# Kernel tuning notes

Measured on AMD Instinct MI355X. Metric: run time of the kernel, lower is better.

Reference implementation:

```python
import jax, jax.numpy as jnp
import numpy as np
from jax import lax

B, L, T = 256, 1024, 128


def setup_inputs() -> dict:
    key = jax.random.key(0)
    k1, k2, k3, k4 = jax.random.split(key, 4)
    transitions = jax.random.normal(k1, (T, T), dtype=jnp.float32)
    feats = jax.random.normal(k2, (B, L, T), dtype=jnp.float32)
    # random lengths in [L//2, L]; position 0 always valid (mask[0].all())
    lengths = jax.random.randint(k3, (B,), L // 2, L + 1)
    mask = jnp.arange(L)[None, :] < lengths[:, None]  # (B, L) bool
    tags = jax.random.randint(k4, (B, L), 0, T).astype(jnp.int64)
    return {"transitions": transitions, "feats": feats, "mask": mask, "tags": tags}


def _forward_score(transitions, feats, mask):
    # CRF forward algorithm: sequential logsumexp DP over time with masking.
    def step(partition, inp):
        f_t, m_t = inp  # (B, T), (B,)
        # scores[b, i, j] = partition[b, i] + transitions[i, j]
        cur = f_t + jax.nn.logsumexp(partition[:, :, None] + transitions[None, :, :], axis=1)
        partition = jnp.where(m_t[:, None], cur, partition)
        return partition, None

    init = feats[:, 0, :]
    feats_t = jnp.swapaxes(feats, 0, 1)  # (L, B, T)
    xs = (feats_t[1:], mask.T[1:])
    partition, _ = lax.scan(step, init, xs)
    return jnp.sum(jax.nn.logsumexp(partition, axis=1))


def _gold_score(transitions, feats, mask, tags):
    unary = jnp.take_along_axis(feats, tags[:, :, None], axis=2)[..., 0]  # (B, L)
    unary_sum = jnp.sum(jnp.where(mask, unary, 0.0))
    binary = transitions[tags[:, :-1], tags[:, 1:]]  # (B, L-1)
    binary_sum = jnp.sum(jnp.where(mask[:, 1:], binary, 0.0))
    return unary_sum + binary_sum


def reference(transitions, feats, mask, tags):
    # scaling_feats == 1 (trainable_balance_weight=False)
    forward_score = _forward_score(transitions, feats, mask)
    gold_score = _gold_score(transitions, feats, mask, tags)
    return forward_score - gold_score
```

## Files before the change

### kernel.cpp

```cpp
#include <hip/hip_runtime.h>

#define CRF_B 256
#define CRF_L 1024
#define CRF_T 128
#define WS_STRIDE 260

typedef __attribute__((ext_vector_type(8))) short bf16x8;
typedef __attribute__((ext_vector_type(4))) float f32x4;
typedef __attribute__((ext_vector_type(2))) short short2v;

#define MF(a, b, cacc) __builtin_amdgcn_mfma_f32_16x16x32_bf16((a), (b), (cacc), 0, 0, 0)
#define WG_BARRIER() asm volatile("s_waitcnt lgkmcnt(0)\n\ts_barrier" ::: "memory")

static __device__ __forceinline__ unsigned short f2bf(float x) {
    union { float f; unsigned u; } v; v.f = x;
    unsigned r = v.u + 0x7FFFu + ((v.u >> 16) & 1u);
    return (unsigned short)(r >> 16);
}
static __device__ __forceinline__ short2v bmax2(short2v a, short2v b) {
    return __builtin_elementwise_max(a, b);
}
static __device__ __forceinline__ short2v fragmax(bf16x8 a) {
    short2v q0 = __builtin_shufflevector(a, a, 0, 1);
    short2v q1 = __builtin_shufflevector(a, a, 2, 3);
    short2v q2 = __builtin_shufflevector(a, a, 4, 5);
    short2v q3 = __builtin_shufflevector(a, a, 6, 7);
    return bmax2(bmax2(q0, q1), bmax2(q2, q3));
}

#define STEP(S, P0, P1, NORM) do {                                             \
    const int sl_ = (S) & 1;                                                   \
    float v0_ = isf ? x0 : F0 * x0;                                            \
    float v1_ = isf ? x1 : F1 * x1;                                            \
    if (g == 0) { s_e[sl_][c0] = f2bf(v0_); s_e[sl_][c1] = f2bf(v1_); }        \
    WG_BARRIER();                                                              \
    bf16x8 A0_ = *(const bf16x8*)&s_e[sl_][ 0 + 8 * g];                        \
    bf16x8 A1_ = *(const bf16x8*)&s_e[sl_][32 + 8 * g];                        \
    bf16x8 A2_ = *(const bf16x8*)&s_e[sl_][64 + 8 * g];                        \
    bf16x8 A3_ = *(const bf16x8*)&s_e[sl_][96 + 8 * g];                        \
    f32x4 dA0_ = MF(A0_, Bf[0][0], Z);  f32x4 dB0_ = MF(A1_, Bf[0][1], Z);     \
    f32x4 dA1_ = MF(A0_, Bf[1][0], Z);  f32x4 dB1_ = MF(A1_, Bf[1][1], Z);     \
    dA0_ = MF(A2_, Bf[0][2], dA0_);  dB0_ = MF(A3_, Bf[0][3], dB0_);           \
    dA1_ = MF(A2_, Bf[1][2], dA1_);  dB1_ = MF(A3_, Bf[1][3], dB1_);           \
    float d0_ = dA0_[0] + dB0_[0];                                             \
    float d1_ = dA1_[0] + dB1_[0];                                             \
    if (NORM) {                                                                \
        short2v mx_ = bmax2(bmax2(fragmax(A0_), fragmax(A1_)),                 \
                            bmax2(fragmax(A2_), fragmax(A3_)));                \
        unsigned mu_ = __builtin_bit_cast(unsigned, mx_);                      \
        float nrm_ = fmaxf(__builtin_bit_cast(float, mu_ << 16),               \
                           __builtin_bit_cast(float, mu_ & 0xFFFF0000u));      \
        float sig_ = __builtin_amdgcn_rcpf(nrm_);                              \
        kap += __logf(nrm_);                                                   \
        d0_ *= sig_; d1_ *= sig_;                                              \
    }                                                                          \
    x0 = isf ? F0 * d0_ : d0_;                                                 \
    x1 = isf ? F1 * d1_ : d1_;                                                 \
    F0 = __expf(P0); F1 = __expf(P1);                                          \
    int rr_ = isf ? ((S) + 3) : (len - (S) - 3);                               \
    if (rr_ > CRF_L - 1) rr_ = CRF_L - 1;                                      \
    if (rr_ < 0) rr_ = 0;                                                      \
    P0 = fb[(size_t)rr_ * CRF_T + c0];                                         \
    P1 = fb[(size_t)rr_ * CRF_T + c1];                                         \
} while (0)

__global__ __launch_bounds__(256, 2) void forward_kernel(
    const float* __restrict__ trans, const float* __restrict__ feats,
    const int* __restrict__ mask, const int* __restrict__ tags,
    float* __restrict__ ws)
{
    const int b    = blockIdx.x >> 1;
    const int dir  = blockIdx.x & 1;
    const bool isf = (dir == 0);
    const int t    = threadIdx.x;
    const int w    = t >> 6;
    const int lane = t & 63;
    const int g    = lane >> 4;
    const int c    = lane & 15;
    const int c0   = 32 * w + c;
    const int c1   = c0 + 16;

    __shared__ __align__(16) unsigned short s_e[2][CRF_T];
    __shared__ float s_gold;
    __shared__ int   s_len;

    if (t == 0) { s_len = 0; s_gold = 0.0f; }
    __syncthreads();

    {
        int cnt = 0; float gsum = 0.0f;
        const int base = b * CRF_L;
        for (int l = t; l < CRF_L; l += 256) {
            if (mask[base + l] != 0) {
                cnt++;
                if (isf) {
                    int tg = tags[base + l];
                    float gv = feats[(size_t)(base + l) * CRF_T + tg];
                    if (l > 0) gv += trans[tags[base + l - 1] * CRF_T + tg];
                    gsum += gv;
                }
            }
        }
        for (int off = 32; off > 0; off >>= 1) {
            cnt  += __shfl_down(cnt, off, 64);
            gsum += __shfl_down(gsum, off, 64);
        }
        if (lane == 0) { atomicAdd(&s_len, cnt); if (isf) atomicAdd(&s_gold, gsum); }
    }

    bf16x8 Bf[2][4];
#pragma unroll
    for (int t2 = 0; t2 < 2; ++t2) {
        const int col = t2 ? c1 : c0;
#pragma unroll
        for (int kt = 0; kt < 4; ++kt)
#pragma unroll
            for (int e = 0; e < 8; ++e) {
                int k = 32 * kt + 8 * g + e;
                int idx = isf ? (k * CRF_T + col) : (col * CRF_T + k);
                Bf[t2][kt][e] = (short)f2bf(__expf(trans[idx]));
            }
    }

    __syncthreads();
    const int len    = s_len;
    const int m      = len >> 1;
    const int nsteps = isf ? m : (len - 1 - m);

    const float* fb = feats + (size_t)b * CRF_L * CRF_T;

    float x0, x1, F0, F1, pfA0, pfA1, pfB0, pfB1;
    float kap = 0.0f;
    if (isf) {
        x0 = __expf(fb[c0]);  x1 = __expf(fb[c1]);
        F0 = __expf(fb[CRF_T + c0]);  F1 = __expf(fb[CRF_T + c1]);
        pfA0 = fb[2 * CRF_T + c0];  pfA1 = fb[2 * CRF_T + c1];
        pfB0 = fb[3 * CRF_T + c0];  pfB1 = fb[3 * CRF_T + c1];
    } else {
        x0 = 1.0f;  x1 = 1.0f;
        F0 = __expf(fb[(size_t)(len - 1) * CRF_T + c0]);
        F1 = __expf(fb[(size_t)(len - 1) * CRF_T + c1]);
        pfA0 = fb[(size_t)(len - 2) * CRF_T + c0];
        pfA1 = fb[(size_t)(len - 2) * CRF_T + c1];
        pfB0 = fb[(size_t)(len - 3) * CRF_T + c0];
        pfB1 = fb[(size_t)(len - 3) * CRF_T + c1];
    }

    const f32x4 Z = {};

    int s = 1;
    for (; s + 1 <= nsteps; s += 2) {
        STEP(s,     pfA0, pfA1, true);
        STEP(s + 1, pfB0, pfB1, false);
    }
    if (s <= nsteps) STEP(s, pfA0, pfA1, true);

    float* wsb = ws + (size_t)b * WS_STRIDE;
    if (g == 0) {
        wsb[dir * 128 + c0] = x0;
        wsb[dir * 128 + c1] = x1;
    }
    if (t == 0) {
        wsb[256 + dir] = kap;
        if (isf) wsb[258] = s_gold;
    }
}

__global__ __launch_bounds__(256) void combine_kernel(
    const float* __restrict__ ws, float* __restrict__ out)
{
    const int t    = threadIdx.x;
    const int lane = t & 63;
    const int w    = t >> 6;
    const float4* pf = (const float4*)(ws + (size_t)t * WS_STRIDE);
    const float4* pb = pf + 32;
    float dot = 0.0f;
#pragma unroll
    for (int k = 0; k < 32; ++k) {
        float4 a = pf[k], bb = pb[k];
        dot += a.x * bb.x + a.y * bb.y + a.z * bb.z + a.w * bb.w;
    }
    const float* ps = ws + (size_t)t * WS_STRIDE;
    float val = ps[256] + ps[257] + __logf(dot) - ps[258];
    for (int off = 32; off > 0; off >>= 1) val += __shfl_down(val, off, 64);
    __shared__ float sw[4];
    if (lane == 0) sw[w] = val;
    __syncthreads();
    if (t == 0) out[0] = sw[0] + sw[1] + sw[2] + sw[3];
}

extern "C" void kernel_launch(void* const* d_in, const int* in_sizes, int n_in,
                              void* d_out, int out_size, void* d_ws, size_t ws_size,
                              hipStream_t stream) {
    const float* trans = (const float*)d_in[0];
    const float* feats = (const float*)d_in[1];
    const int*   mask  = (const int*)d_in[2];
    const int*   tags  = (const int*)d_in[3];
    float*       out   = (float*)d_out;
    float*       ws    = (float*)d_ws;

    hipLaunchKernelGGL(forward_kernel, dim3(2 * CRF_B), dim3(256), 0, stream,
                       trans, feats, mask, tags, ws);
    hipLaunchKernelGGL(combine_kernel, dim3(1), dim3(256), 0, stream, ws, out);
}
```

Measured before the change: 184.4 us.

## Batch eight sequences per block so MFMA rows carry multiple batch elements

```diff
diff --git a/kernel.cpp b/kernel.cpp
--- a/kernel.cpp
+++ b/kernel.cpp
@@ -3,13 +3,13 @@
 #define CRF_B 256
 #define CRF_L 1024
 #define CRF_T 128
-#define WS_STRIDE 260
+#define BPB   8
+#define WS_STRIDE 264
 
 typedef __attribute__((ext_vector_type(8))) short bf16x8;
 typedef __attribute__((ext_vector_type(4))) float f32x4;
-typedef __attribute__((ext_vector_type(2))) short short2v;
-
-#define MF(a, b, cacc) __builtin_amdgcn_mfma_f32_16x16x32_bf16((a), (b), (cacc), 0, 0, 0)
+
+#define MF(a, b, c_) __builtin_amdgcn_mfma_f32_16x16x32_bf16((a), (b), (c_), 0, 0, 0)
 #define WG_BARRIER() asm volatile("s_waitcnt lgkmcnt(0)\n\ts_barrier" ::: "memory")
 
 static __device__ __forceinline__ unsigned short f2bf(float x) {
@@ -17,80 +17,129 @@
     unsigned r = v.u + 0x7FFFu + ((v.u >> 16) & 1u);
     return (unsigned short)(r >> 16);
 }
-static __device__ __forceinline__ short2v bmax2(short2v a, short2v b) {
-    return __builtin_elementwise_max(a, b);
-}
-static __device__ __forceinline__ short2v fragmax(bf16x8 a) {
-    short2v q0 = __builtin_shufflevector(a, a, 0, 1);
-    short2v q1 = __builtin_shufflevector(a, a, 2, 3);
-    short2v q2 = __builtin_shufflevector(a, a, 4, 5);
-    short2v q3 = __builtin_shufflevector(a, a, 6, 7);
-    return bmax2(bmax2(q0, q1), bmax2(q2, q3));
-}
-
-#define STEP(S, P0, P1, NORM) do {                                             \
-    const int sl_ = (S) & 1;                                                   \
-    float v0_ = isf ? x0 : F0 * x0;                                            \
-    float v1_ = isf ? x1 : F1 * x1;                                            \
-    if (g == 0) { s_e[sl_][c0] = f2bf(v0_); s_e[sl_][c1] = f2bf(v1_); }        \
+
+static __device__ __forceinline__ float rowmax16(float v) {
+    int x;
+    x = __builtin_amdgcn_update_dpp(0, __builtin_bit_cast(int, v), 0xB1,  0xF, 0xF, true);
+    v = fmaxf(v, __builtin_bit_cast(float, x));
+    x = __builtin_amdgcn_update_dpp(0, __builtin_bit_cast(int, v), 0x4E,  0xF, 0xF, true);
+    v = fmaxf(v, __builtin_bit_cast(float, x));
+    x = __builtin_amdgcn_update_dpp(0, __builtin_bit_cast(int, v), 0x141, 0xF, 0xF, true);
+    v = fmaxf(v, __builtin_bit_cast(float, x));
+    x = __builtin_amdgcn_update_dpp(0, __builtin_bit_cast(int, v), 0x140, 0xF, 0xF, true);
+    v = fmaxf(v, __builtin_bit_cast(float, x));
+    return v;
+}
+
+#define STEP(S, PF, DONORM) do {                                               \
+    const int  sl_ = (S) & 1;                                                  \
+    char* xb_ = s_xraw + sl_ * 4096;                                           \
+    float F0_[4], F1_[4];                                                      \
+    _Pragma("unroll")                                                          \
+    for (int r_ = 0; r_ < 4; ++r_) {                                           \
+        F0_[r_] = __expf(PF[r_].x);                                            \
+        F1_[r_] = __expf(PF[r_].y);                                            \
+    }                                                                          \
+    if (g2 < 2) {                                                              \
+        _Pragma("unroll")                                                      \
+        for (int r_ = 0; r_ < 4; ++r_) {                                       \
+            const int row_ = 4 * g2 + r_;                                      \
+            float p0_ = isf ? x0[r_] : F0_[r_] * x0[r_];                       \
+            float p1_ = isf ? x1[r_] : F1_[r_] * x1[r_];                       \
+            unsigned pk_ = (__builtin_bit_cast(unsigned, p1_) & 0xFFFF0000u)   \
+                         | (__builtin_bit_cast(unsigned, p0_) >> 16);          \
+            *(unsigned*)(xb_ + row_ * 256 + ((tg0 * 2) ^ (row_ << 4))) = pk_;  \
+        }                                                                      \
+    }                                                                          \
+    _Pragma("unroll")                                                          \
+    for (int r_ = 0; r_ < 4; ++r_) {                                           \
+        int la_ = isf ? (off[r_] + 4 * 512) : (off[r_] - 4 * 512);             \
+        if (!isf) la_ = (la_ < base0[r_]) ? base0[r_] : la_;                   \
+        PF[r_] = *(const float2*)(fbc + la_);                                  \
+        off[r_] += isf ? 512 : -512;                                           \
+    }                                                                          \
     WG_BARRIER();                                                              \
-    bf16x8 A0_ = *(const bf16x8*)&s_e[sl_][ 0 + 8 * g];                        \
-    bf16x8 A1_ = *(const bf16x8*)&s_e[sl_][32 + 8 * g];                        \
-    bf16x8 A2_ = *(const bf16x8*)&s_e[sl_][64 + 8 * g];                        \
-    bf16x8 A3_ = *(const bf16x8*)&s_e[sl_][96 + 8 * g];                        \
+    const char* xr_ = xb_ + c * 256;                                           \
+    bf16x8 A0_ = *(const bf16x8*)(xr_ + ((  0 + 16 * g2) ^ ((c & 7) << 4)));   \
+    bf16x8 A1_ = *(const bf16x8*)(xr_ + (( 64 + 16 * g2) ^ ((c & 7) << 4)));   \
+    bf16x8 A2_ = *(const bf16x8*)(xr_ + ((128 + 16 * g2) ^ ((c & 7) << 4)));   \
+    bf16x8 A3_ = *(const bf16x8*)(xr_ + ((192 + 16 * g2) ^ ((c & 7) << 4)));   \
     f32x4 dA0_ = MF(A0_, Bf[0][0], Z);  f32x4 dB0_ = MF(A1_, Bf[0][1], Z);     \
     f32x4 dA1_ = MF(A0_, Bf[1][0], Z);  f32x4 dB1_ = MF(A1_, Bf[1][1], Z);     \
     dA0_ = MF(A2_, Bf[0][2], dA0_);  dB0_ = MF(A3_, Bf[0][3], dB0_);           \
     dA1_ = MF(A2_, Bf[1][2], dA1_);  dB1_ = MF(A3_, Bf[1][3], dB1_);           \
-    float d0_ = dA0_[0] + dB0_[0];                                             \
-    float d1_ = dA1_[0] + dB1_[0];                                             \
-    if (NORM) {                                                                \
-        short2v mx_ = bmax2(bmax2(fragmax(A0_), fragmax(A1_)),                 \
-                            bmax2(fragmax(A2_), fragmax(A3_)));                \
-        unsigned mu_ = __builtin_bit_cast(unsigned, mx_);                      \
-        float nrm_ = fmaxf(__builtin_bit_cast(float, mu_ << 16),               \
-                           __builtin_bit_cast(float, mu_ & 0xFFFF0000u));      \
-        float sig_ = __builtin_amdgcn_rcpf(nrm_);                              \
-        kap += __logf(nrm_);                                                   \
-        d0_ *= sig_; d1_ *= sig_;                                              \
-    }                                                                          \
-    x0 = isf ? F0 * d0_ : d0_;                                                 \
-    x1 = isf ? F1 * d1_ : d1_;                                                 \
-    F0 = __expf(P0); F1 = __expf(P1);                                          \
-    int rr_ = isf ? ((S) + 3) : (len - (S) - 3);                               \
-    if (rr_ > CRF_L - 1) rr_ = CRF_L - 1;                                      \
-    if (rr_ < 0) rr_ = 0;                                                      \
-    P0 = fb[(size_t)rr_ * CRF_T + c0];                                         \
-    P1 = fb[(size_t)rr_ * CRF_T + c1];                                         \
+    if (DONORM) {                                                              \
+        const int pp_ = ((S) >> 1) & 1;                                        \
+        const float* pm_ = s_pm + (pp_ ^ 1) * 32 + (g2 & 1) * 4;               \
+        f32x4 n0_ = *(const f32x4*)(pm_ + 0);                                  \
+        f32x4 n1_ = *(const f32x4*)(pm_ + 8);                                  \
+        f32x4 n2_ = *(const f32x4*)(pm_ + 16);                                 \
+        f32x4 n3_ = *(const f32x4*)(pm_ + 24);                                 \
+        _Pragma("unroll")                                                      \
+        for (int r_ = 0; r_ < 4; ++r_) {                                       \
+            float nr_ = fmaxf(fmaxf(n0_[r_], n1_[r_]), fmaxf(n2_[r_], n3_[r_]));\
+            float sg_ = __builtin_amdgcn_rcpf(nr_);                            \
+            kap[r_] += __logf(nr_);                                            \
+            float d0_ = (dA0_[r_] + dB0_[r_]) * sg_;                           \
+            float d1_ = (dA1_[r_] + dB1_[r_]) * sg_;                           \
+            x0[r_] = isf ? F0_[r_] * d0_ : d0_;                                \
+            x1[r_] = isf ? F1_[r_] * d1_ : d1_;                                \
+        }                                                                      \
+    } else {                                                                   \
+        _Pragma("unroll")                                                      \
+        for (int r_ = 0; r_ < 4; ++r_) {                                       \
+            float d0_ = dA0_[r_] + dB0_[r_];                                   \
+            float d1_ = dA1_[r_] + dB1_[r_];                                   \
+            x0[r_] = isf ? F0_[r_] * d0_ : d0_;                                \
+            x1[r_] = isf ? F1_[r_] * d1_ : d1_;                                \
+        }                                                                      \
+    }                                                                          \
+    _Pragma("unroll")                                                          \
+    for (int r_ = 0; r_ < 4; ++r_) {                                           \
+        bool hit_ = ((S) == msv[r_]);                                          \
+        sv0[r_] = hit_ ? x0[r_] : sv0[r_];                                     \
+        sv1[r_] = hit_ ? x1[r_] : sv1[r_];                                     \
+        svk[r_] = hit_ ? kap[r_] : svk[r_];                                    \
+    }                                                                          \
+    if (DONORM) {                                                              \
+        const int pp_ = ((S) >> 1) & 1;                                        \
+        float pmx_[4];                                                         \
+        _Pragma("unroll")                                                      \
+        for (int r_ = 0; r_ < 4; ++r_)                                         \
+            pmx_[r_] = rowmax16(fmaxf(x0[r_], x1[r_]));                        \
+        if (c == 0 && g2 < 2) {                                                \
+            f32x4 pv_; pv_[0]=pmx_[0]; pv_[1]=pmx_[1]; pv_[2]=pmx_[2]; pv_[3]=pmx_[3]; \
+            *(f32x4*)(s_pm + pp_ * 32 + w * 8 + g2 * 4) = pv_;                 \
+        }                                                                      \
+    }                                                                          \
 } while (0)
 
-__global__ __launch_bounds__(256, 2) void forward_kernel(
+__global__ __launch_bounds__(256, 1) void forward_kernel(
     const float* __restrict__ trans, const float* __restrict__ feats,
     const int* __restrict__ mask, const int* __restrict__ tags,
     float* __restrict__ ws)
 {
-    const int b    = blockIdx.x >> 1;
+    const int bg   = blockIdx.x >> 1;
     const int dir  = blockIdx.x & 1;
     const bool isf = (dir == 0);
     const int t    = threadIdx.x;
     const int w    = t >> 6;
     const int lane = t & 63;
-    const int g    = lane >> 4;
+    const int g2   = lane >> 4;
     const int c    = lane & 15;
-    const int c0   = 32 * w + c;
-    const int c1   = c0 + 16;
-
-    __shared__ __align__(16) unsigned short s_e[2][CRF_T];
-    __shared__ float s_gold;
-    __shared__ int   s_len;
-
-    if (t == 0) { s_len = 0; s_gold = 0.0f; }
-    __syncthreads();
+    const int tg0  = 32 * w + 2 * c;
+
+    __shared__ __align__(16) char  s_xraw[2 * 4096];
+    __shared__ __align__(16) float s_pm[64];
+    __shared__ int   s_len8[BPB];
+    __shared__ float s_gold8[BPB];
 
     {
+        const int q  = t >> 5;
+        const int i0 = t & 31;
         int cnt = 0; float gsum = 0.0f;
-        const int base = b * CRF_L;
-        for (int l = t; l < CRF_L; l += 256) {
+        const int base = (bg * BPB + q) * CRF_L;
+        for (int l = i0; l < CRF_L; l += 32) {
             if (mask[base + l] != 0) {
                 cnt++;
                 if (isf) {
@@ -101,68 +150,103 @@
                 }
             }
         }
-        for (int off = 32; off > 0; off >>= 1) {
-            cnt  += __shfl_down(cnt, off, 64);
-            gsum += __shfl_down(gsum, off, 64);
-        }
-        if (lane == 0) { atomicAdd(&s_len, cnt); if (isf) atomicAdd(&s_gold, gsum); }
+        for (int o = 16; o > 0; o >>= 1) {
+            cnt  += __shfl_xor(cnt, o, 64);
+            gsum += __shfl_xor(gsum, o, 64);
+        }
+        if (i0 == 0) { s_len8[q] = cnt; s_gold8[q] = gsum; }
+    }
+
+    {
+        unsigned* zp = (unsigned*)s_xraw;
+        for (int i = t; i < 2048; i += 256) {
+            int buf = i >> 10, word = i & 1023;
+            if (word >= 512) zp[buf * 1024 + word] = 0u;
+        }
+        if (t < 64) s_pm[t] = 1.0f;
     }
 
     bf16x8 Bf[2][4];
 #pragma unroll
     for (int t2 = 0; t2 < 2; ++t2) {
-        const int col = t2 ? c1 : c0;
+        const int col = tg0 + t2;
 #pragma unroll
         for (int kt = 0; kt < 4; ++kt)
 #pragma unroll
             for (int e = 0; e < 8; ++e) {
-                int k = 32 * kt + 8 * g + e;
+                int k = 32 * kt + 8 * g2 + e;
                 int idx = isf ? (k * CRF_T + col) : (col * CRF_T + k);
                 Bf[t2][kt][e] = (short)f2bf(__expf(trans[idx]));
             }
     }
 
     __syncthreads();
-    const int len    = s_len;
-    const int m      = len >> 1;
-    const int nsteps = isf ? m : (len - 1 - m);
-
-    const float* fb = feats + (size_t)b * CRF_L * CRF_T;
-
-    float x0, x1, F0, F1, pfA0, pfA1, pfB0, pfB1;
-    float kap = 0.0f;
-    if (isf) {
-        x0 = __expf(fb[c0]);  x1 = __expf(fb[c1]);
-        F0 = __expf(fb[CRF_T + c0]);  F1 = __expf(fb[CRF_T + c1]);
-        pfA0 = fb[2 * CRF_T + c0];  pfA1 = fb[2 * CRF_T + c1];
-        pfB0 = fb[3 * CRF_T + c0];  pfB1 = fb[3 * CRF_T + c1];
-    } else {
-        x0 = 1.0f;  x1 = 1.0f;
-        F0 = __expf(fb[(size_t)(len - 1) * CRF_T + c0]);
-        F1 = __expf(fb[(size_t)(len - 1) * CRF_T + c1]);
-        pfA0 = fb[(size_t)(len - 2) * CRF_T + c0];
-        pfA1 = fb[(size_t)(len - 2) * CRF_T + c1];
-        pfB0 = fb[(size_t)(len - 3) * CRF_T + c0];
-        pfB1 = fb[(size_t)(len - 3) * CRF_T + c1];
+
+    int nsteps = 0;
+#pragma unroll
+    for (int qq = 0; qq < BPB; ++qq) {
+        int L_ = s_len8[qq];
+        int ns_ = isf ? (L_ >> 1) : ((L_ - 1) >> 1);
+        nsteps = (ns_ > nsteps) ? ns_ : nsteps;
+    }
+
+    const char* fbc = (const char*)feats;
+    int msv[4], off[4], base0[4];
+    float x0[4], x1[4], kap[4], sv0[4], sv1[4], svk[4];
+    float2 pfA[4], pfB[4], pfC[4], pfD[4];
+
+#pragma unroll
+    for (int r = 0; r < 4; ++r) {
+        const int qi = 4 * (g2 & 1) + r;
+        const int qb = bg * BPB + qi;
+        const int len = s_len8[qi];
+        msv[r]   = isf ? (len >> 1) : ((len - 1) >> 1);
+        base0[r] = qb * (CRF_L * CRF_T * 4) + tg0 * 4;
+        kap[r] = 0.0f;
+        if (isf) {
+            float2 v0 = *(const float2*)(fbc + base0[r]);
+            x0[r] = __expf(v0.x); x1[r] = __expf(v0.y);
+            off[r] = base0[r] + 512;
+            pfA[r] = *(const float2*)(fbc + off[r]);
+            pfB[r] = *(const float2*)(fbc + off[r] + 512);
+            pfC[r] = *(const float2*)(fbc + off[r] + 1024);
+            pfD[r] = *(const float2*)(fbc + off[r] + 1536);
+        } else {
+            x0[r] = 1.0f; x1[r] = 1.0f;
+            off[r] = base0[r] + (len - 1) * 512;
+            pfA[r] = *(const float2*)(fbc + off[r]);
+            pfB[r] = *(const float2*)(fbc + off[r] - 512);
+            pfC[r] = *(const float2*)(fbc + off[r] - 1024);
+            pfD[r] = *(const float2*)(fbc + off[r] - 1536);
+        }
+        sv0[r] = x0[r]; sv1[r] = x1[r]; svk[r] = 0.0f;
     }
 
     const f32x4 Z = {};
 
+    const int lim = 1 + (nsteps & ~3);
     int s = 1;
-    for (; s + 1 <= nsteps; s += 2) {
-        STEP(s,     pfA0, pfA1, true);
-        STEP(s + 1, pfB0, pfB1, false);
-    }
-    if (s <= nsteps) STEP(s, pfA0, pfA1, true);
-
-    float* wsb = ws + (size_t)b * WS_STRIDE;
-    if (g == 0) {
-        wsb[dir * 128 + c0] = x0;
-        wsb[dir * 128 + c1] = x1;
-    }
-    if (t == 0) {
-        wsb[256 + dir] = kap;
-        if (isf) wsb[258] = s_gold;
+    for (; s < lim; s += 4) {
+        STEP(s,     pfA, true);
+        STEP(s + 1, pfB, false);
+        STEP(s + 2, pfC, true);
+        STEP(s + 3, pfD, false);
+    }
+    if (s <= nsteps) { STEP(s, pfA, true);  s++; }
+    if (s <= nsteps) { STEP(s, pfB, false); s++; }
+    if (s <= nsteps) { STEP(s, pfC, true); }
+
+    if (g2 < 2) {
+#pragma unroll
+        for (int r = 0; r < 4; ++r) {
+            const int qb = bg * BPB + 4 * g2 + r;
+            float2 vv; vv.x = sv0[r]; vv.y = sv1[r];
+            *(float2*)(ws + (size_t)qb * WS_STRIDE + dir * 128 + tg0) = vv;
+            if (c == 0 && w == 0) {
+                ws[(size_t)qb * WS_STRIDE + 256 + dir] = svk[r];
+                if (isf) ws[(size_t)qb * WS_STRIDE + 258] = s_gold8[4 * g2 + r];
+            }
+        }
     }
 }
 
@@ -182,7 +266,7 @@
     }
     const float* ps = ws + (size_t)t * WS_STRIDE;
     float val = ps[256] + ps[257] + __logf(dot) - ps[258];
-    for (int off = 32; off > 0; off >>= 1) val += __shfl_down(val, off, 64);
+    for (int o = 32; o > 0; o >>= 1) val += __shfl_down(val, o, 64);
     __shared__ float sw[4];
     if (lane == 0) sw[w] = val;
     __syncthreads();
@@ -199,7 +283,7 @@
     float*       out   = (float*)d_out;
     float*       ws    = (float*)d_ws;
 
-    hipLaunchKernelGGL(forward_kernel, dim3(2 * CRF_B), dim3(256), 0, stream,
+    hipLaunchKernelGGL(forward_kernel, dim3(2 * CRF_B / BPB), dim3(256), 0, stream,
                        trans, feats, mask, tags, ws);
     hipLaunchKernelGGL(combine_kernel, dim3(1), dim3(256), 0, stream, ws, out);
 }
```

Result: slower. 346.2 us (+87.7%).

## Use two-wave blocks with four MFMA columns per lane and per-step deferred normalization

Applied to the files above, without the earlier changes.

```diff
diff --git a/kernel.cpp b/kernel.cpp
--- a/kernel.cpp
+++ b/kernel.cpp
@@ -3,19 +3,23 @@
 #define CRF_B 256
 #define CRF_L 1024
 #define CRF_T 128
-#define WS_STRIDE 260
+#define WS_STRIDE 264
 
 typedef __attribute__((ext_vector_type(8))) short bf16x8;
 typedef __attribute__((ext_vector_type(4))) float f32x4;
 typedef __attribute__((ext_vector_type(2))) short short2v;
 
-#define MF(a, b, cacc) __builtin_amdgcn_mfma_f32_16x16x32_bf16((a), (b), (cacc), 0, 0, 0)
+#define MF(a, b, c_) __builtin_amdgcn_mfma_f32_16x16x32_bf16((a), (b), (c_), 0, 0, 0)
 #define WG_BARRIER() asm volatile("s_waitcnt lgkmcnt(0)\n\ts_barrier" ::: "memory")
 
 static __device__ __forceinline__ unsigned short f2bf(float x) {
     union { float f; unsigned u; } v; v.f = x;
     unsigned r = v.u + 0x7FFFu + ((v.u >> 16) & 1u);
     return (unsigned short)(r >> 16);
+}
+static __device__ __forceinline__ unsigned pack2(float a, float b) {
+    return (__builtin_bit_cast(unsigned, b) & 0xFFFF0000u) |
+           (__builtin_bit_cast(unsigned, a) >> 16);
 }
 static __device__ __forceinline__ short2v bmax2(short2v a, short2v b) {
     return __builtin_elementwise_max(a, b);
@@ -28,43 +32,56 @@
     return bmax2(bmax2(q0, q1), bmax2(q2, q3));
 }
 
-#define STEP(S, P0, P1, NORM) do {                                             \
-    const int sl_ = (S) & 1;                                                   \
-    float v0_ = isf ? x0 : F0 * x0;                                            \
-    float v1_ = isf ? x1 : F1 * x1;                                            \
-    if (g == 0) { s_e[sl_][c0] = f2bf(v0_); s_e[sl_][c1] = f2bf(v1_); }        \
-    WG_BARRIER();                                                              \
-    bf16x8 A0_ = *(const bf16x8*)&s_e[sl_][ 0 + 8 * g];                        \
-    bf16x8 A1_ = *(const bf16x8*)&s_e[sl_][32 + 8 * g];                        \
-    bf16x8 A2_ = *(const bf16x8*)&s_e[sl_][64 + 8 * g];                        \
-    bf16x8 A3_ = *(const bf16x8*)&s_e[sl_][96 + 8 * g];                        \
-    f32x4 dA0_ = MF(A0_, Bf[0][0], Z);  f32x4 dB0_ = MF(A1_, Bf[0][1], Z);     \
-    f32x4 dA1_ = MF(A0_, Bf[1][0], Z);  f32x4 dB1_ = MF(A1_, Bf[1][1], Z);     \
-    dA0_ = MF(A2_, Bf[0][2], dA0_);  dB0_ = MF(A3_, Bf[0][3], dB0_);           \
-    dA1_ = MF(A2_, Bf[1][2], dA1_);  dB1_ = MF(A3_, Bf[1][3], dB1_);           \
-    float d0_ = dA0_[0] + dB0_[0];                                             \
-    float d1_ = dA1_[0] + dB1_[0];                                             \
-    if (NORM) {                                                                \
-        short2v mx_ = bmax2(bmax2(fragmax(A0_), fragmax(A1_)),                 \
-                            bmax2(fragmax(A2_), fragmax(A3_)));                \
-        unsigned mu_ = __builtin_bit_cast(unsigned, mx_);                      \
-        float nrm_ = fmaxf(__builtin_bit_cast(float, mu_ << 16),               \
-                           __builtin_bit_cast(float, mu_ & 0xFFFF0000u));      \
-        float sig_ = __builtin_amdgcn_rcpf(nrm_);                              \
-        kap += __logf(nrm_);                                                   \
-        d0_ *= sig_; d1_ *= sig_;                                              \
-    }                                                                          \
-    x0 = isf ? F0 * d0_ : d0_;                                                 \
-    x1 = isf ? F1 * d1_ : d1_;                                                 \
-    F0 = __expf(P0); F1 = __expf(P1);                                          \
-    int rr_ = isf ? ((S) + 3) : (len - (S) - 3);                               \
-    if (rr_ > CRF_L - 1) rr_ = CRF_L - 1;                                      \
-    if (rr_ < 0) rr_ = 0;                                                      \
-    P0 = fb[(size_t)rr_ * CRF_T + c0];                                         \
-    P1 = fb[(size_t)rr_ * CRF_T + c1];                                         \
+#define STEP(PFv) do {                                                        \
+    kap += lognrm;                                                            \
+    float Fs0_ = Fcur[0]*sig, Fs1_ = Fcur[1]*sig,                             \
+          Fs2_ = Fcur[2]*sig, Fs3_ = Fcur[3]*sig;                             \
+    if (g2 == 0) {                                                            \
+        unsigned lo_, hi_;                                                    \
+        if (isf) { lo_ = pack2(x[0], x[1]); hi_ = pack2(x[2], x[3]); }        \
+        else     { lo_ = pack2(Fs0_*x[0], Fs1_*x[1]);                         \
+                   hi_ = pack2(Fs2_*x[2], Fs3_*x[3]); }                       \
+        *(unsigned long long*)(s_x + sloff + 128*W + 8*c) =                   \
+            ((unsigned long long)hi_ << 32) | lo_;                            \
+    }                                                                         \
+    _Pragma("unroll")                                                         \
+    for (int m_ = 0; m_ < 4; ++m_) {                                          \
+        Fcur[m_] = __expf(PFv[m_]);                                           \
+        PFv[m_]  = *(const float*)(fptr + fcol[m_]);                          \
+    }                                                                         \
+    fptr += fstep;                                                            \
+    WG_BARRIER();                                                             \
+    const char* xr_ = s_x + sloff;                                            \
+    bf16x8 A0_ = *(const bf16x8*)(xr_ +   0 + 16*g2);                         \
+    bf16x8 A1_ = *(const bf16x8*)(xr_ +  64 + 16*g2);                         \
+    bf16x8 A2_ = *(const bf16x8*)(xr_ + 128 + 16*g2);                         \
+    bf16x8 A3_ = *(const bf16x8*)(xr_ + 192 + 16*g2);                         \
+    sloff ^= 256;                                                             \
+    f32x4 p0a = MF(A0_, Bf[0][0], Z); f32x4 p0b = MF(A1_, Bf[0][1], Z);       \
+    f32x4 p1a = MF(A0_, Bf[1][0], Z); f32x4 p1b = MF(A1_, Bf[1][1], Z);       \
+    f32x4 p2a = MF(A0_, Bf[2][0], Z); f32x4 p2b = MF(A1_, Bf[2][1], Z);       \
+    f32x4 p3a = MF(A0_, Bf[3][0], Z); f32x4 p3b = MF(A1_, Bf[3][1], Z);       \
+    p0a = MF(A2_, Bf[0][2], p0a); p0b = MF(A3_, Bf[0][3], p0b);               \
+    p1a = MF(A2_, Bf[1][2], p1a); p1b = MF(A3_, Bf[1][3], p1b);               \
+    p2a = MF(A2_, Bf[2][2], p2a); p2b = MF(A3_, Bf[2][3], p2b);               \
+    p3a = MF(A2_, Bf[3][2], p3a); p3b = MF(A3_, Bf[3][3], p3b);               \
+    float d0_ = p0a[0] + p0b[0], d1_ = p1a[0] + p1b[0];                       \
+    float d2_ = p2a[0] + p2b[0], d3_ = p3a[0] + p3b[0];                       \
+    if (isf) { x[0] = Fs0_*d0_; x[1] = Fs1_*d1_;                              \
+               x[2] = Fs2_*d2_; x[3] = Fs3_*d3_; }                            \
+    else     { x[0] = d0_; x[1] = d1_; x[2] = d2_; x[3] = d3_; }              \
+    short2v mx_ = bmax2(bmax2(fragmax(A0_), fragmax(A1_)),                    \
+                        bmax2(fragmax(A2_), fragmax(A3_)));                   \
+    unsigned mu_ = __builtin_bit_cast(unsigned, mx_);                         \
+    float nm_ = fmaxf(__builtin_bit_cast(float, mu_ << 16),                   \
+                      __builtin_bit_cast(float, mu_ & 0xFFFF0000u));          \
+    nm_ = fmaxf(nm_, __shfl_xor(nm_, 16, 64));                                \
+    nm_ = fmaxf(nm_, __shfl_xor(nm_, 32, 64));                                \
+    sig    = __builtin_amdgcn_rcpf(nm_);                                      \
+    lognrm = __logf(nm_);                                                     \
 } while (0)
 
-__global__ __launch_bounds__(256, 2) void forward_kernel(
+__global__ __launch_bounds__(128, 1) void forward_kernel(
     const float* __restrict__ trans, const float* __restrict__ feats,
     const int* __restrict__ mask, const int* __restrict__ tags,
     float* __restrict__ ws)
@@ -73,16 +90,14 @@
     const int dir  = blockIdx.x & 1;
     const bool isf = (dir == 0);
     const int t    = threadIdx.x;
-    const int w    = t >> 6;
+    const int W    = t >> 6;
     const int lane = t & 63;
-    const int g    = lane >> 4;
+    const int g2   = lane >> 4;
     const int c    = lane & 15;
-    const int c0   = 32 * w + c;
-    const int c1   = c0 + 16;
-
-    __shared__ __align__(16) unsigned short s_e[2][CRF_T];
+
+    __shared__ __align__(16) char s_x[512];
+    __shared__ int   s_len;
     __shared__ float s_gold;
-    __shared__ int   s_len;
 
     if (t == 0) { s_len = 0; s_gold = 0.0f; }
     __syncthreads();
@@ -90,7 +105,7 @@
     {
         int cnt = 0; float gsum = 0.0f;
         const int base = b * CRF_L;
-        for (int l = t; l < CRF_L; l += 256) {
+        for (int l = t; l < CRF_L; l += 128) {
             if (mask[base + l] != 0) {
                 cnt++;
                 if (isf) {
@@ -101,69 +116,81 @@
                 }
             }
         }
-        for (int off = 32; off > 0; off >>= 1) {
-            cnt  += __shfl_down(cnt, off, 64);
-            gsum += __shfl_down(gsum, off, 64);
+        for (int o = 32; o > 0; o >>= 1) {
+            cnt  += __shfl_down(cnt, o, 64);
+            gsum += __shfl_down(gsum, o, 64);
         }
         if (lane == 0) { atomicAdd(&s_len, cnt); if (isf) atomicAdd(&s_gold, gsum); }
     }
 
-    bf16x8 Bf[2][4];
-#pragma unroll
-    for (int t2 = 0; t2 < 2; ++t2) {
-        const int col = t2 ? c1 : c0;
+    bf16x8 Bf[4][4];
+#pragma unroll
+    for (int m = 0; m < 4; ++m) {
+        const int col = 64 * W + 16 * m + c;
 #pragma unroll
         for (int kt = 0; kt < 4; ++kt)
 #pragma unroll
             for (int e = 0; e < 8; ++e) {
-                int k = 32 * kt + 8 * g + e;
-                int idx = isf ? (k * CRF_T + col) : (col * CRF_T + k);
-                Bf[t2][kt][e] = (short)f2bf(__expf(trans[idx]));
+                int pos  = 32 * kt + 8 * g2 + e;
+                int ktag = 64 * (pos >> 6) + 16 * (pos & 3) + ((pos >> 2) & 15);
+                int idx  = isf ? (ktag * CRF_T + col) : (col * CRF_T + ktag);
+                Bf[m][kt][e] = (short)f2bf(__expf(trans[idx]));
             }
     }
 
     __syncthreads();
     const int len    = s_len;
-    const int m      = len >> 1;
-    const int nsteps = isf ? m : (len - 1 - m);
-
-    const float* fb = feats + (size_t)b * CRF_L * CRF_T;
-
-    float x0, x1, F0, F1, pfA0, pfA1, pfB0, pfB1;
-    float kap = 0.0f;
+    const int mmid   = len >> 1;
+    const int nsteps = isf ? mmid : (len - 1 - mmid);
+
+    const char* fb = (const char*)feats + (size_t)b * CRF_L * CRF_T * 4;
+    int fcol[4];
+#pragma unroll
+    for (int m = 0; m < 4; ++m) fcol[m] = (64 * W + 16 * m + c) * 4;
+#define ROWP(r) (fb + (size_t)(r) * 512)
+
+    float x[4], Fcur[4], pfA[4], pfB[4], pfC[4], pfD[4];
+    float kap = 0.0f, sig = 1.0f, lognrm = 0.0f;
+
     if (isf) {
-        x0 = __expf(fb[c0]);  x1 = __expf(fb[c1]);
-        F0 = __expf(fb[CRF_T + c0]);  F1 = __expf(fb[CRF_T + c1]);
-        pfA0 = fb[2 * CRF_T + c0];  pfA1 = fb[2 * CRF_T + c1];
-        pfB0 = fb[3 * CRF_T + c0];  pfB1 = fb[3 * CRF_T + c1];
+#pragma unroll
+        for (int m = 0; m < 4; ++m) {
+            x[m]    = __expf(*(const float*)(ROWP(0) + fcol[m]));
+            Fcur[m] = __expf(*(const float*)(ROWP(1) + fcol[m]));
+            pfA[m]  = *(const float*)(ROWP(2) + fcol[m]);
+            pfB[m]  = *(const float*)(ROWP(3) + fcol[m]);
+            pfC[m]  = *(const float*)(ROWP(4) + fcol[m]);
+            pfD[m]  = *(const float*)(ROWP(5) + fcol[m]);
+        }
     } else {
-        x0 = 1.0f;  x1 = 1.0f;
-        F0 = __expf(fb[(size_t)(len - 1) * CRF_T + c0]);
-        F1 = __expf(fb[(size_t)(len - 1) * CRF_T + c1]);
-        pfA0 = fb[(size_t)(len - 2) * CRF_T + c0];
-        pfA1 = fb[(size_t)(len - 2) * CRF_T + c1];
-        pfB0 = fb[(size_t)(len - 3) * CRF_T + c0];
-        pfB1 = fb[(size_t)(len - 3) * CRF_T + c1];
-    }
-
+#pragma unroll
+        for (int m = 0; m < 4; ++m) {
+            x[m]    = 1.0f;
+            Fcur[m] = __expf(*(const float*)(ROWP(len - 1) + fcol[m]));
+            pfA[m]  = *(const float*)(ROWP(len - 2) + fcol[m]);
+            pfB[m]  = *(const float*)(ROWP(len - 3) + fcol[m]);
+            pfC[m]  = *(const float*)(ROWP(len - 4) + fcol[m]);
+            pfD[m]  = *(const float*)(ROWP(len - 5) + fcol[m]);
+        }
+    }
+    const char* fptr = isf ? ROWP(6) : ROWP(len - 6);
+    const int   fstep = isf ? 512 : -512;
+    unsigned sloff = 0;
     const f32x4 Z = {};
 
-    int s = 1;
-    for (; s + 1 <= nsteps; s += 2) {
-        STEP(s,     pfA0, pfA1, true);
-        STEP(s + 1, pfB0, pfB1, false);
-    }
-    if (s <= nsteps) STEP(s, pfA0, pfA1, true);
+    int s = 0;
+    for (; s + 4 <= nsteps; s += 4) { STEP(pfA); STEP(pfB); STEP(pfC); STEP(pfD); }
+    if (s < nsteps) { STEP(pfA); s++; }
+    if (s < nsteps) { STEP(pfB); s++; }
+    if (s < nsteps) { STEP(pfC); }
 
     float* wsb = ws + (size_t)b * WS_STRIDE;
-    if (g == 0) {
-        wsb[dir * 128 + c0] = x0;
-        wsb[dir * 128 + c1] = x1;
-    }
-    if (t == 0) {
-        wsb[256 + dir] = kap;
-        if (isf) wsb[258] = s_gold;
-    }
+    if (g2 == 0) {
+#pragma unroll
+        for (int m = 0; m < 4; ++m)
+            wsb[dir * 128 + 64 * W + 16 * m + c] = x[m];
+    }
+    if (t == 0) { wsb[256 + dir] = kap; if (isf) wsb[258] = s_gold; }
 }
 
 __global__ __launch_bounds__(256) void combine_kernel(
@@ -182,7 +209,7 @@
     }
     const float* ps = ws + (size_t)t * WS_STRIDE;
     float val = ps[256] + ps[257] + __logf(dot) - ps[258];
-    for (int off = 32; off > 0; off >>= 1) val += __shfl_down(val, off, 64);
+    for (int o = 32; o > 0; o >>= 1) val += __shfl_down(val, o, 64);
     __shared__ float sw[4];
     if (lane == 0) sw[w] = val;
     __syncthreads();
@@ -199,7 +226,7 @@
     float*       out   = (float*)d_out;
     float*       ws    = (float*)d_ws;
 
-    hipLaunchKernelGGL(forward_kernel, dim3(2 * CRF_B), dim3(256), 0, stream,
+    hipLaunchKernelGGL(forward_kernel, dim3(2 * CRF_B), dim3(128), 0, stream,
                        trans, feats, mask, tags, ws);
     hipLaunchKernelGGL(combine_kernel, dim3(1), dim3(256), 0, stream, ws, out);
 }
```

Measured after the change: 311.1 us. +68.7%, slower.

## Run each CRF chain direction in a single wavefront, interleaving two batches

Applied to the files above, without the earlier changes.

```diff
diff --git a/kernel.cpp b/kernel.cpp
--- a/kernel.cpp
+++ b/kernel.cpp
@@ -3,166 +3,202 @@
 #define CRF_B 256
 #define CRF_L 1024
 #define CRF_T 128
-#define WS_STRIDE 260
+#define WS_STRIDE 264
 
 typedef __attribute__((ext_vector_type(8))) short bf16x8;
 typedef __attribute__((ext_vector_type(4))) float f32x4;
+typedef __attribute__((ext_vector_type(4))) unsigned u32x4;
 typedef __attribute__((ext_vector_type(2))) short short2v;
 
-#define MF(a, b, cacc) __builtin_amdgcn_mfma_f32_16x16x32_bf16((a), (b), (cacc), 0, 0, 0)
-#define WG_BARRIER() asm volatile("s_waitcnt lgkmcnt(0)\n\ts_barrier" ::: "memory")
+#define MF(a, b, c_) __builtin_amdgcn_mfma_f32_16x16x32_bf16((a), (b), (c_), 0, 0, 0)
 
 static __device__ __forceinline__ unsigned short f2bf(float x) {
     union { float f; unsigned u; } v; v.f = x;
     unsigned r = v.u + 0x7FFFu + ((v.u >> 16) & 1u);
     return (unsigned short)(r >> 16);
 }
+static __device__ __forceinline__ unsigned pack2(float a, float b) {
+    return (__builtin_bit_cast(unsigned, b) & 0xFFFF0000u) |
+           (__builtin_bit_cast(unsigned, a) >> 16);
+}
 static __device__ __forceinline__ short2v bmax2(short2v a, short2v b) {
     return __builtin_elementwise_max(a, b);
 }
-static __device__ __forceinline__ short2v fragmax(bf16x8 a) {
-    short2v q0 = __builtin_shufflevector(a, a, 0, 1);
-    short2v q1 = __builtin_shufflevector(a, a, 2, 3);
-    short2v q2 = __builtin_shufflevector(a, a, 4, 5);
-    short2v q3 = __builtin_shufflevector(a, a, 6, 7);
-    return bmax2(bmax2(q0, q1), bmax2(q2, q3));
-}
-
-#define STEP(S, P0, P1, NORM) do {                                             \
-    const int sl_ = (S) & 1;                                                   \
-    float v0_ = isf ? x0 : F0 * x0;                                            \
-    float v1_ = isf ? x1 : F1 * x1;                                            \
-    if (g == 0) { s_e[sl_][c0] = f2bf(v0_); s_e[sl_][c1] = f2bf(v1_); }        \
-    WG_BARRIER();                                                              \
-    bf16x8 A0_ = *(const bf16x8*)&s_e[sl_][ 0 + 8 * g];                        \
-    bf16x8 A1_ = *(const bf16x8*)&s_e[sl_][32 + 8 * g];                        \
-    bf16x8 A2_ = *(const bf16x8*)&s_e[sl_][64 + 8 * g];                        \
-    bf16x8 A3_ = *(const bf16x8*)&s_e[sl_][96 + 8 * g];                        \
-    f32x4 dA0_ = MF(A0_, Bf[0][0], Z);  f32x4 dB0_ = MF(A1_, Bf[0][1], Z);     \
-    f32x4 dA1_ = MF(A0_, Bf[1][0], Z);  f32x4 dB1_ = MF(A1_, Bf[1][1], Z);     \
-    dA0_ = MF(A2_, Bf[0][2], dA0_);  dB0_ = MF(A3_, Bf[0][3], dB0_);           \
-    dA1_ = MF(A2_, Bf[1][2], dA1_);  dB1_ = MF(A3_, Bf[1][3], dB1_);           \
-    float d0_ = dA0_[0] + dB0_[0];                                             \
-    float d1_ = dA1_[0] + dB1_[0];                                             \
-    if (NORM) {                                                                \
-        short2v mx_ = bmax2(bmax2(fragmax(A0_), fragmax(A1_)),                 \
-                            bmax2(fragmax(A2_), fragmax(A3_)));                \
-        unsigned mu_ = __builtin_bit_cast(unsigned, mx_);                      \
-        float nrm_ = fmaxf(__builtin_bit_cast(float, mu_ << 16),               \
-                           __builtin_bit_cast(float, mu_ & 0xFFFF0000u));      \
-        float sig_ = __builtin_amdgcn_rcpf(nrm_);                              \
-        kap += __logf(nrm_);                                                   \
-        d0_ *= sig_; d1_ *= sig_;                                              \
+static __device__ __forceinline__ short2v u2s(unsigned w) {
+    return __builtin_bit_cast(short2v, w);
+}
+
+#define STEP_CH(S, X, FC, PF, KAP, SIG, LN, NS, LEN, FBP, DONORM) do {         \
+    const bool up_ = (S) <= (NS);                                              \
+    (KAP) += up_ ? (LN) : 0.0f;                                                \
+    unsigned pk0_, pk1_, pk2_, pk3_;                                           \
+    if (isf) {                                                                 \
+        pk0_ = pack2(X[0], X[1]); pk1_ = pack2(X[2], X[3]);                    \
+        pk2_ = pack2(X[4], X[5]); pk3_ = pack2(X[6], X[7]);                    \
+    } else {                                                                   \
+        pk0_ = pack2(FC[0]*(SIG)*X[0], FC[1]*(SIG)*X[1]);                      \
+        pk1_ = pack2(FC[2]*(SIG)*X[2], FC[3]*(SIG)*X[3]);                      \
+        pk2_ = pack2(FC[4]*(SIG)*X[4], FC[5]*(SIG)*X[5]);                      \
+        pk3_ = pack2(FC[6]*(SIG)*X[6], FC[7]*(SIG)*X[7]);                      \
     }                                                                          \
-    x0 = isf ? F0 * d0_ : d0_;                                                 \
-    x1 = isf ? F1 * d1_ : d1_;                                                 \
-    F0 = __expf(P0); F1 = __expf(P1);                                          \
-    int rr_ = isf ? ((S) + 3) : (len - (S) - 3);                               \
-    if (rr_ > CRF_L - 1) rr_ = CRF_L - 1;                                      \
-    if (rr_ < 0) rr_ = 0;                                                      \
-    P0 = fb[(size_t)rr_ * CRF_T + c0];                                         \
-    P1 = fb[(size_t)rr_ * CRF_T + c1];                                         \
+    unsigned w00_=__shfl(pk0_,sl0,64), w01_=__shfl(pk0_,sl1,64),               \
+             w02_=__shfl(pk0_,sl2,64), w03_=__shfl(pk0_,sl3,64);               \
+    unsigned w10_=__shfl(pk1_,sl0,64), w11_=__shfl(pk1_,sl1,64),               \
+             w12_=__shfl(pk1_,sl2,64), w13_=__shfl(pk1_,sl3,64);               \
+    unsigned w20_=__shfl(pk2_,sl0,64), w21_=__shfl(pk2_,sl1,64),               \
+             w22_=__shfl(pk2_,sl2,64), w23_=__shfl(pk2_,sl3,64);               \
+    unsigned w30_=__shfl(pk3_,sl0,64), w31_=__shfl(pk3_,sl1,64),               \
+             w32_=__shfl(pk3_,sl2,64), w33_=__shfl(pk3_,sl3,64);               \
+    u32x4 q0_ = {w00_, w01_, w02_, w03_};                                      \
+    u32x4 q1_ = {w10_, w11_, w12_, w13_};                                      \
+    u32x4 q2_ = {w20_, w21_, w22_, w23_};                                      \
+    u32x4 q3_ = {w30_, w31_, w32_, w33_};                                      \
+    bf16x8 A0_ = __builtin_bit_cast(bf16x8, q0_);                              \
+    bf16x8 A1_ = __builtin_bit_cast(bf16x8, q1_);                              \
+    bf16x8 A2_ = __builtin_bit_cast(bf16x8, q2_);                              \
+    bf16x8 A3_ = __builtin_bit_cast(bf16x8, q3_);                              \
+    f32x4 ac_[8];                                                              \
+    _Pragma("unroll") for (int m_ = 0; m_ < 8; ++m_) ac_[m_] = MF(A0_, Bf[m_][0], Z);        \
+    _Pragma("unroll") for (int m_ = 0; m_ < 8; ++m_) ac_[m_] = MF(A1_, Bf[m_][1], ac_[m_]);  \
+    _Pragma("unroll") for (int m_ = 0; m_ < 8; ++m_) ac_[m_] = MF(A2_, Bf[m_][2], ac_[m_]);  \
+    _Pragma("unroll") for (int m_ = 0; m_ < 8; ++m_) ac_[m_] = MF(A3_, Bf[m_][3], ac_[m_]);  \
+    _Pragma("unroll") for (int m_ = 0; m_ < 8; ++m_) {                         \
+        float xn_ = isf ? (FC[m_] * (SIG)) * ac_[m_][0] : ac_[m_][0];          \
+        X[m_] = up_ ? xn_ : X[m_];                                             \
+    }                                                                          \
+    { int r_ = isf ? ((S) + 3) : ((LEN) - (S) - 3);                            \
+      r_ = r_ < 0 ? 0 : (r_ > CRF_L - 1 ? CRF_L - 1 : r_);                     \
+      const float* rp_ = (FBP) + (size_t)r_ * CRF_T;                           \
+      _Pragma("unroll") for (int m_ = 0; m_ < 8; ++m_) {                       \
+          FC[m_] = __expf(PF[m_]); PF[m_] = rp_[16 * m_ + c]; } }              \
+    if (DONORM) {                                                              \
+        short2v t0_ = bmax2(bmax2(u2s(w00_), u2s(w01_)), bmax2(u2s(w02_), u2s(w03_)));  \
+        short2v t1_ = bmax2(bmax2(u2s(w10_), u2s(w11_)), bmax2(u2s(w12_), u2s(w13_)));  \
+        short2v t2_ = bmax2(bmax2(u2s(w20_), u2s(w21_)), bmax2(u2s(w22_), u2s(w23_)));  \
+        short2v t3_ = bmax2(bmax2(u2s(w30_), u2s(w31_)), bmax2(u2s(w32_), u2s(w33_)));  \
+        short2v tm_ = bmax2(bmax2(t0_, t1_), bmax2(t2_, t3_));                 \
+        unsigned mu_ = __builtin_bit_cast(unsigned, tm_);                      \
+        float nm_ = fmaxf(__builtin_bit_cast(float, mu_ << 16),                \
+                          __builtin_bit_cast(float, mu_ & 0xFFFF0000u));       \
+        nm_ = fmaxf(nm_, __shfl_xor(nm_, 16, 64));                             \
+        nm_ = fmaxf(nm_, __shfl_xor(nm_, 32, 64));                             \
+        (SIG) = __builtin_amdgcn_rcpf(nm_); (LN) = __logf(nm_);                \
+    } else { (SIG) = 1.0f; (LN) = 0.0f; }                                      \
 } while (0)
 
-__global__ __launch_bounds__(256, 2) void forward_kernel(
+__global__ __launch_bounds__(256, 1) void forward_kernel(
     const float* __restrict__ trans, const float* __restrict__ feats,
     const int* __restrict__ mask, const int* __restrict__ tags,
     float* __restrict__ ws)
 {
-    const int b    = blockIdx.x >> 1;
-    const int dir  = blockIdx.x & 1;
+    const int t    = threadIdx.x;
+    const int gw   = blockIdx.x * 4 + (t >> 6);
+    const int dir  = gw & 1;
     const bool isf = (dir == 0);
-    const int t    = threadIdx.x;
-    const int w    = t >> 6;
+    const int bA   = gw >> 1;
+    const int bB   = bA + 128;
     const int lane = t & 63;
-    const int g    = lane >> 4;
+    const int g2   = lane >> 4;
     const int c    = lane & 15;
-    const int c0   = 32 * w + c;
-    const int c1   = c0 + 16;
-
-    __shared__ __align__(16) unsigned short s_e[2][CRF_T];
-    __shared__ float s_gold;
-    __shared__ int   s_len;
-
-    if (t == 0) { s_len = 0; s_gold = 0.0f; }
-    __syncthreads();
-
+    const int sl0  = 4 * g2, sl1 = sl0 + 1, sl2 = sl0 + 2, sl3 = sl0 + 3;
+
+    int lenA = 0, lenB = 0; float goldA = 0.0f, goldB = 0.0f;
     {
-        int cnt = 0; float gsum = 0.0f;
-        const int base = b * CRF_L;
-        for (int l = t; l < CRF_L; l += 256) {
-            if (mask[base + l] != 0) {
-                cnt++;
-                if (isf) {
-                    int tg = tags[base + l];
-                    float gv = feats[(size_t)(base + l) * CRF_T + tg];
-                    if (l > 0) gv += trans[tags[base + l - 1] * CRF_T + tg];
-                    gsum += gv;
-                }
+        const int baA = bA * CRF_L, baB = bB * CRF_L;
+        for (int l = lane; l < CRF_L; l += 64) {
+            int mA = mask[baA + l], mB = mask[baB + l];
+            lenA += (mA != 0); lenB += (mB != 0);
+            if (isf) {
+                if (mA) { int tg = tags[baA + l];
+                    float gv = feats[(size_t)(baA + l) * CRF_T + tg];
+                    if (l > 0) gv += trans[tags[baA + l - 1] * CRF_T + tg];
+                    goldA += gv; }
+                if (mB) { int tg = tags[baB + l];
+                    float gv = feats[(size_t)(baB + l) * CRF_T + tg];
+                    if (l > 0) gv += trans[tags[baB + l - 1] * CRF_T + tg];
+                    goldB += gv; }
             }
         }
-        for (int off = 32; off > 0; off >>= 1) {
-            cnt  += __shfl_down(cnt, off, 64);
-            gsum += __shfl_down(gsum, off, 64);
-        }
-        if (lane == 0) { atomicAdd(&s_len, cnt); if (isf) atomicAdd(&s_gold, gsum); }
-    }
-
-    bf16x8 Bf[2][4];
-#pragma unroll
-    for (int t2 = 0; t2 < 2; ++t2) {
-        const int col = t2 ? c1 : c0;
+#pragma unroll
+        for (int o = 32; o > 0; o >>= 1) {
+            lenA += __shfl_xor(lenA, o, 64); lenB += __shfl_xor(lenB, o, 64);
+            goldA += __shfl_xor(goldA, o, 64); goldB += __shfl_xor(goldB, o, 64);
+        }
+    }
+
+    bf16x8 Bf[8][4];
+#pragma unroll
+    for (int m = 0; m < 8; ++m) {
+        const int col = 16 * m + c;
 #pragma unroll
         for (int kt = 0; kt < 4; ++kt)
 #pragma unroll
             for (int e = 0; e < 8; ++e) {
-                int k = 32 * kt + 8 * g + e;
-                int idx = isf ? (k * CRF_T + col) : (col * CRF_T + k);
-                Bf[t2][kt][e] = (short)f2bf(__expf(trans[idx]));
+                int tag = 16 * (2 * kt + (e & 1)) + (4 * g2 + (e >> 1));
+                int idx = isf ? (tag * CRF_T + col) : (col * CRF_T + tag);
+                Bf[m][kt][e] = (short)f2bf(__expf(trans[idx]));
             }
     }
 
-    __syncthreads();
-    const int len    = s_len;
-    const int m      = len >> 1;
-    const int nsteps = isf ? m : (len - 1 - m);
-
-    const float* fb = feats + (size_t)b * CRF_L * CRF_T;
-
-    float x0, x1, F0, F1, pfA0, pfA1, pfB0, pfB1;
-    float kap = 0.0f;
+    const float* fbA = feats + (size_t)bA * CRF_L * CRF_T;
+    const float* fbB = feats + (size_t)bB * CRF_L * CRF_T;
+    float xA[8], FcA[8], pfA[8], xB[8], FcB[8], pfB[8];
+    float kapA = 0.0f, sigA = 1.0f, lnA = 0.0f;
+    float kapB = 0.0f, sigB = 1.0f, lnB = 0.0f;
+    int nsA, nsB;
     if (isf) {
-        x0 = __expf(fb[c0]);  x1 = __expf(fb[c1]);
-        F0 = __expf(fb[CRF_T + c0]);  F1 = __expf(fb[CRF_T + c1]);
-        pfA0 = fb[2 * CRF_T + c0];  pfA1 = fb[2 * CRF_T + c1];
-        pfB0 = fb[3 * CRF_T + c0];  pfB1 = fb[3 * CRF_T + c1];
+        nsA = lenA >> 1;  nsB = lenB >> 1;
+#pragma unroll
+        for (int m = 0; m < 8; ++m) {
+            xA[m]  = __expf(fbA[16 * m + c]);
+            FcA[m] = __expf(fbA[CRF_T + 16 * m + c]);
+            pfA[m] = fbA[2 * CRF_T + 16 * m + c];
+            xB[m]  = __expf(fbB[16 * m + c]);
+            FcB[m] = __expf(fbB[CRF_T + 16 * m + c]);
+            pfB[m] = fbB[2 * CRF_T + 16 * m + c];
+        }
     } else {
-        x0 = 1.0f;  x1 = 1.0f;
-        F0 = __expf(fb[(size_t)(len - 1) * CRF_T + c0]);
-        F1 = __expf(fb[(size_t)(len - 1) * CRF_T + c1]);
-        pfA0 = fb[(size_t)(len - 2) * CRF_T + c0];
-        pfA1 = fb[(size_t)(len - 2) * CRF_T + c1];
-        pfB0 = fb[(size_t)(len - 3) * CRF_T + c0];
-        pfB1 = fb[(size_t)(len - 3) * CRF_T + c1];
-    }
-
+        nsA = lenA - 1 - (lenA >> 1);  nsB = lenB - 1 - (lenB >> 1);
+#pragma unroll
+        for (int m = 0; m < 8; ++m) {
+            xA[m]  = 1.0f;
+            FcA[m] = __expf(fbA[(size_t)(lenA - 1) * CRF_T + 16 * m + c]);
+            pfA[m] = fbA[(size_t)(lenA - 2) * CRF_T + 16 * m + c];
+            xB[m]  = 1.0f;
+            FcB[m] = __expf(fbB[(size_t)(lenB - 1) * CRF_T + 16 * m + c]);
+            pfB[m] = fbB[(size_t)(lenB - 2) * CRF_T + 16 * m + c];
+        }
+    }
+
+    const int maxns = nsA > nsB ? nsA : nsB;
     const f32x4 Z = {};
 
     int s = 1;
-    for (; s + 1 <= nsteps; s += 2) {
-        STEP(s,     pfA0, pfA1, true);
-        STEP(s + 1, pfB0, pfB1, false);
-    }
-    if (s <= nsteps) STEP(s, pfA0, pfA1, true);
-
-    float* wsb = ws + (size_t)b * WS_STRIDE;
-    if (g == 0) {
-        wsb[dir * 128 + c0] = x0;
-        wsb[dir * 128 + c1] = x1;
-    }
-    if (t == 0) {
-        wsb[256 + dir] = kap;
-        if (isf) wsb[258] = s_gold;
+    for (; s + 1 <= maxns; s += 2) {
+        STEP_CH(s,     xA, FcA, pfA, kapA, sigA, lnA, nsA, lenA, fbA, true);
+        STEP_CH(s,     xB, FcB, pfB, kapB, sigB, lnB, nsB, lenB, fbB, true);
+        STEP_CH(s + 1, xA, FcA, pfA, kapA, sigA, lnA, nsA, lenA, fbA, false);
+        STEP_CH(s + 1, xB, FcB, pfB, kapB, sigB, lnB, nsB, lenB, fbB, false);
+    }
+    if (s <= maxns) {
+        STEP_CH(s, xA, FcA, pfA, kapA, sigA, lnA, nsA, lenA, fbA, true);
+        STEP_CH(s, xB, FcB, pfB, kapB, sigB, lnB, nsB, lenB, fbB, true);
+    }
+
+    if (g2 == 0) {
+#pragma unroll
+        for (int m = 0; m < 8; ++m) {
+            ws[(size_t)bA * WS_STRIDE + dir * 128 + 16 * m + c] = xA[m];
+            ws[(size_t)bB * WS_STRIDE + dir * 128 + 16 * m + c] = xB[m];
+        }
+    }
+    if (lane == 0) {
+        ws[(size_t)bA * WS_STRIDE + 256 + dir] = kapA;
+        ws[(size_t)bB * WS_STRIDE + 256 + dir] = kapB;
+        if (isf) {
+            ws[(size_t)bA * WS_STRIDE + 258] = goldA;
+            ws[(size_t)bB * WS_STRIDE + 258] = goldB;
+        }
     }
 }
 
@@ -182,7 +218,7 @@
     }
     const float* ps = ws + (size_t)t * WS_STRIDE;
     float val = ps[256] + ps[257] + __logf(dot) - ps[258];
-    for (int off = 32; off > 0; off >>= 1) val += __shfl_down(val, off, 64);
+    for (int o = 32; o > 0; o >>= 1) val += __shfl_down(val, o, 64);
     __shared__ float sw[4];
     if (lane == 0) sw[w] = val;
     __syncthreads();
@@ -199,7 +235,7 @@
     float*       out   = (float*)d_out;
     float*       ws    = (float*)d_ws;
 
-    hipLaunchKernelGGL(forward_kernel, dim3(2 * CRF_B), dim3(256), 0, stream,
+    hipLaunchKernelGGL(forward_kernel, dim3(64), dim3(256), 0, stream,
                        trans, feats, mask, tags, ws);
     hipLaunchKernelGGL(combine_kernel, dim3(1), dim3(256), 0, stream, ws, out);
 }
```

New measurement: 602.5 us. +226.7%, slower.
